# Kernel tuning notes

Measured on AMD Instinct MI355X. Metric: run time of the kernel, lower is better.

Reference implementation:

```python
import jax, jax.numpy as jnp
import numpy as np

B, L, E, H, WINDOW = 4, 1024, 1024, 16, 4
D = E // H  # head_dim = 64
SCALING = D ** -0.5


def setup_inputs() -> dict:
    key = jax.random.key(0)
    ks = jax.random.split(key, 12)
    s = E ** -0.5
    return {
        "hidden_states": jax.random.normal(ks[0], (B, L, E), dtype=jnp.float32),
        "Wq": jax.random.normal(ks[1], (E, E), dtype=jnp.float32) * s,
        "bq": jnp.zeros((E,), dtype=jnp.float32),
        "Wk": jax.random.normal(ks[2], (E, E), dtype=jnp.float32) * s,
        "bk": jnp.zeros((E,), dtype=jnp.float32),
        "Wv": jax.random.normal(ks[3], (E, E), dtype=jnp.float32) * s,
        "bv": jnp.zeros((E,), dtype=jnp.float32),
        "Wo": jax.random.normal(ks[4], (E, E), dtype=jnp.float32) * s,
        "bo": jnp.zeros((E,), dtype=jnp.float32),
        "emb_rel_k": jax.random.normal(ks[5], (1, 2 * WINDOW + 1, D), dtype=jnp.float32) * SCALING,
        "emb_rel_v": jax.random.normal(ks[6], (1, 2 * WINDOW + 1, D), dtype=jnp.float32) * SCALING,
    }


def _get_relative_embeddings(emb, length):
    # emb: (1, 2*window+1, D) -> (1, 2*length-1, D)
    pad_length = max(length - (WINDOW + 1), 0)
    if pad_length > 0:
        emb = jnp.pad(emb, ((0, 0), (pad_length, pad_length), (0, 0)))
    start = max(WINDOW + 1 - length, 0)
    return emb[:, start:start + 2 * length - 1]


def _rel_to_abs(x):
    # x: (BH, L, 2L-1) -> (BH, L, L)
    bh, length, _ = x.shape
    x = jnp.pad(x, ((0, 0), (0, 0), (0, 1)))            # (BH, L, 2L)
    xf = x.reshape(bh, length * 2 * length)
    xf = jnp.pad(xf, ((0, 0), (0, length - 1)))
    xfin = xf.reshape(bh, length + 1, 2 * length - 1)
    return xfin[:, :length, length - 1:]


def _abs_to_rel(x):
    # x: (BH, L, L) -> (BH, L, 2L-1)
    bh, length, _ = x.shape
    x = jnp.pad(x, ((0, 0), (0, 0), (0, length - 1)))    # (BH, L, 2L-1)
    xf = x.reshape(bh, length * (2 * length - 1))
    xf = jnp.pad(xf, ((0, 0), (length, 0)))
    xfin = xf.reshape(bh, length, 2 * length)
    return xfin[:, :, 1:]


def reference(hidden_states, Wq, bq, Wk, bk, Wv, bv, Wo, bo, emb_rel_k, emb_rel_v):
    bsz, tgt_len, _ = hidden_states.shape

    def shape(t):  # (B, L, E) -> (B*H, L, D)
        return t.reshape(bsz, tgt_len, H, D).transpose(0, 2, 1, 3).reshape(bsz * H, tgt_len, D)

    q = shape((hidden_states @ Wq + bq) * SCALING)
    k = shape(hidden_states @ Wk + bk)
    v = shape(hidden_states @ Wv + bv)
    src_len = k.shape[1]

    attn_weights = jnp.einsum("btd,bsd->bts", q, k)  # (BH, L, L)

    rel_k = _get_relative_embeddings(emb_rel_k, src_len)          # (1, 2L-1, D)
    rel_logits = jnp.einsum("btd,md->btm", q, rel_k[0])           # (BH, L, 2L-1)
    attn_weights = attn_weights + _rel_to_abs(rel_logits)

    attn_probs = jax.nn.softmax(attn_weights, axis=-1)

    attn_output = jnp.einsum("bts,bsd->btd", attn_probs, v)       # (BH, L, D)

    rel_v = _get_relative_embeddings(emb_rel_v, src_len)          # (1, 2L-1, D)
    rel_weights = _abs_to_rel(attn_probs)                         # (BH, L, 2L-1)
    attn_output = attn_output + jnp.einsum("btm,md->btd", rel_weights, rel_v[0])

    out = attn_output.reshape(bsz, H, tgt_len, D).transpose(0, 2, 1, 3).reshape(bsz, tgt_len, E)
    return out @ Wo + bo
```

## Files before the change

### kernel.cpp

```cpp
#include <hip/hip_runtime.h>
#include <math.h>

#define LQ 1024
#define EE 1024
#define NH 16
#define HD 64
#define SCALING 0.125f

typedef unsigned short u16;
typedef __bf16 bf16x8 __attribute__((ext_vector_type(8)));
typedef __bf16 bf16x4 __attribute__((ext_vector_type(4)));
typedef float f32x4 __attribute__((ext_vector_type(4)));

#define MFMA16(a, b, c) __builtin_amdgcn_mfma_f32_16x16x32_bf16(a, b, c, 0, 0, 0)
#define BAR() __builtin_amdgcn_s_barrier()

__device__ __forceinline__ void split_bf16(float x, __bf16& h, __bf16& l)
{
    h = (__bf16)x;
    l = (__bf16)(x - (float)h);
}

__device__ __forceinline__ u16 bf16_bits(__bf16 v)
{
    union { __bf16 b; u16 u; } cv;
    cv.b = v;
    return cv.u;
}

__global__ __launch_bounds__(256) void conv_all(
    const float* __restrict__ A,
    const float* __restrict__ Wq, const float* __restrict__ Wk,
    const float* __restrict__ Wv, const float* __restrict__ Wo,
    __bf16* __restrict__ Ah,
    __bf16* __restrict__ BTq, __bf16* __restrict__ BTk,
    __bf16* __restrict__ BTv, __bf16* __restrict__ BTo)
{
    __shared__ float tbuf[64][65];
    const int bid = blockIdx.x;
    const int tid = threadIdx.x;

    if (bid < 1024) {
        int t = bid * 256 + tid;
#pragma unroll
        for (int it = 0; it < 4; it++) {
            int f = t + it * 262144;
            int m = f >> 8, c4 = f & 255;
            float4 x = ((const float4*)A)[f];
            bf16x4 hv;
            hv[0] = (__bf16)x.x; hv[1] = (__bf16)x.y;
            hv[2] = (__bf16)x.z; hv[3] = (__bf16)x.w;
            *(bf16x4*)(Ah + (size_t)m * 1024 + c4 * 4) = hv;
        }
        return;
    }

    const int b2 = bid - 1024;
    const int z  = b2 >> 8;
    const int rem = b2 & 255;
    const int n0 = (rem & 15) * 64, k0 = (rem >> 4) * 64;
    const float* W = (z == 0) ? Wq : (z == 1) ? Wk : (z == 2) ? Wv : Wo;
    __bf16* BT     = (z == 0) ? BTq : (z == 1) ? BTk : (z == 2) ? BTv : BTo;

#pragma unroll
    for (int rr = 0; rr < 4; rr++) {
        int f = rr * 256 + tid;
        int kl = f >> 4, n4 = f & 15;
        float4 x = *(const float4*)&W[(size_t)(k0 + kl) * EE + n0 + n4 * 4];
        tbuf[kl][n4 * 4 + 0] = x.x;
        tbuf[kl][n4 * 4 + 1] = x.y;
        tbuf[kl][n4 * 4 + 2] = x.z;
        tbuf[kl][n4 * 4 + 3] = x.w;
    }
    __syncthreads();
#pragma unroll
    for (int rr = 0; rr < 2; rr++) {
        int f = rr * 256 + tid;
        int nl = f >> 3, c8 = f & 7;
        bf16x8 hv;
#pragma unroll
        for (int j = 0; j < 8; j++) hv[j] = (__bf16)tbuf[c8 * 8 + j][nl];
        *(bf16x8*)(BT + (size_t)(n0 + nl) * 1024 + k0 + c8 * 8) = hv;
    }
}

__global__ __launch_bounds__(512, 2) void qkv_mfma(
    const u16* __restrict__ Ah, const u16* __restrict__ BTall,
    const float* __restrict__ bq, const float* __restrict__ bk, const float* __restrict__ bv,
    __bf16* __restrict__ qo, __bf16* __restrict__ ko, __bf16* __restrict__ vto)
{
    const int wg   = blockIdx.x;
    const int xcd  = wg & 7, idx = wg >> 3;
    const int tile = xcd * 24 + idx;
    const int by   = tile / 12, bx = tile % 12;

    __shared__ __attribute__((aligned(16))) u16 smem[65536];
    u16 (*Ab_lds)[2][8192] = (u16(*)[2][8192])smem;
    u16 (*Bb_lds)[2][8192] = (u16(*)[2][8192])(smem + 32768);

    const int tid  = threadIdx.x;
    const int lane = tid & 63;
    const int wave = tid >> 6;
    const int wr   = wave >> 2, wc = wave & 3;
    const int rl   = lane & 15, lq = lane >> 4;

    const int m0    = by * 256;
    const int nrow0 = bx * 256;

    f32x4 acc[8][4] = {};
    bf16x8 af[2][4], bn0[2][2], bn1[2][2];

    auto stA = [&](int buf, int half, int kt) {
        int k0 = kt * 64;
#pragma unroll
        for (int it = 0; it < 2; it++) {
            int c = it * 512 + tid, k2 = c >> 7, row = c & 127;
            __builtin_amdgcn_global_load_lds(
                Ah + (size_t)(m0 + half * 128 + row) * 1024 + k0 + k2 * 8,
                &Ab_lds[buf][half][c * 8], 16, 0, 0);
        }
    };
    auto stB = [&](int buf, int half, int kt) {
        int k0 = kt * 64;
#pragma unroll
        for (int it = 0; it < 2; it++) {
            int c = it * 512 + tid, k2 = c >> 7, row = c & 127;
            __builtin_amdgcn_global_load_lds(
                BTall + (size_t)(nrow0 + half * 128 + row) * 1024 + k0 + k2 * 8,
                &Bb_lds[buf][half][c * 8], 16, 0, 0);
        }
    };
    auto rdA = [&](int buf, int mh) {
#pragma unroll
        for (int kk = 0; kk < 2; kk++)
#pragma unroll
            for (int mi = 0; mi < 4; mi++)
                af[kk][mi] = *(const bf16x8*)&Ab_lds[buf][wr]
                    [((kk * 4 + lq) * 128 + mh * 64 + mi * 16 + rl) * 8];
    };
    auto rdB = [&](int buf, int nh, bf16x8 (&bf)[2][2]) {
#pragma unroll
        for (int kk = 0; kk < 2; kk++)
#pragma unroll
            for (int ni = 0; ni < 2; ni++)
                bf[kk][ni] = *(const bf16x8*)&Bb_lds[buf][wc >> 1]
                    [((kk * 4 + lq) * 128 + (wc & 1) * 64 + nh * 32 + ni * 16 + rl) * 8];
    };
    auto mfma_q = [&](int mh, int nh, bf16x8 (&bf)[2][2]) {
        __builtin_amdgcn_s_setprio(1);
#pragma unroll
        for (int kk = 0; kk < 2; kk++)
#pragma unroll
            for (int mi = 0; mi < 4; mi++)
#pragma unroll
                for (int ni = 0; ni < 2; ni++)
                    acc[mh * 4 + mi][nh * 2 + ni] =
                        MFMA16(af[kk][mi], bf[kk][ni], acc[mh * 4 + mi][nh * 2 + ni]);
        __builtin_amdgcn_s_setprio(0);
    };

    auto body = [&](int t, bool last) {
        rdA(0, 0); rdB(0, 0, bn0);
        stA(1, 0, t + 1);
        BAR(); mfma_q(0, 0, bn0); BAR();
        rdB(0, 1, bn1);
        stA(1, 1, t + 1);
        BAR(); mfma_q(0, 1, bn1); BAR();
        rdA(0, 1);
        if (!last) stB(0, 0, t + 2);
        BAR(); mfma_q(1, 0, bn0); BAR();
        if (!last) {
            stB(0, 1, t + 2);
            asm volatile("s_waitcnt vmcnt(4)" ::: "memory");
        } else {
            asm volatile("s_waitcnt vmcnt(0)" ::: "memory");
        }
        BAR(); mfma_q(1, 1, bn1); BAR();
        rdA(1, 0); rdB(1, 0, bn0);
        if (!last) stA(0, 0, t + 2);
        BAR(); mfma_q(0, 0, bn0); BAR();
        rdB(1, 1, bn1);
        if (!last) stA(0, 1, t + 2);
        BAR(); mfma_q(0, 1, bn1); BAR();
        rdA(1, 1);
        if (!last) stB(1, 0, t + 3);
        BAR(); mfma_q(1, 0, bn0); BAR();
        if (!last) {
            stB(1, 1, t + 3);
            asm volatile("s_waitcnt vmcnt(4)" ::: "memory");
        }
        BAR(); mfma_q(1, 1, bn1); BAR();
    };

    stB(0, 0, 0); stB(0, 1, 0);
    stA(0, 0, 0); stA(0, 1, 0);
    stB(1, 0, 1); stB(1, 1, 1);
    asm volatile("s_waitcnt vmcnt(4)" ::: "memory");
    BAR();

    for (int i = 0; i < 7; i++) body(2 * i, false);
    body(14, true);

    const int z   = bx >> 2;
    const int n0l = (bx & 3) * 256;
    const float* bias = (z == 0) ? bq : (z == 1) ? bk : bv;
    const float qs    = (z == 0) ? SCALING : 1.0f;
    const int b  = m0 >> 10;
    const int t0 = m0 & 1023;

    if (z < 2) {
        __bf16* O = (z == 0) ? qo : ko;
#pragma unroll
        for (int mi = 0; mi < 8; mi++)
#pragma unroll
            for (int ni = 0; ni < 4; ni++) {
                int col = wc * 64 + ni * 16 + rl;
                float bb = bias[n0l + col];
                int c = col >> 3, j = col & 7;
#pragma unroll
                for (int r = 0; r < 4; r++) {
                    int row = wr * 128 + mi * 16 + lq * 4 + r;
                    smem[((row << 5) + (c ^ (row & 15))) * 8 + j] =
                        bf16_bits((__bf16)((acc[mi][ni][r] + bb) * qs));
                }
            }
        __syncthreads();
        const int h0 = n0l >> 6;
#pragma unroll
        for (int it = 0; it < 16; it++) {
            int id = it * 512 + tid;
            int row = id >> 5, c = id & 31;
            bf16x8 vv = *(const bf16x8*)&smem[((row << 5) + (c ^ (row & 15))) * 8];
            __bf16* dst = O + ((size_t)((b * NH + h0 + (c >> 3)) * LQ) + t0 + row) * HD
                            + (c & 7) * 8;
            *(bf16x8*)dst = vv;
        }
    } else {
#pragma unroll
        for (int mi = 0; mi < 8; mi++)
#pragma unroll
            for (int ni = 0; ni < 4; ni++) {
                int n = n0l + wc * 64 + ni * 16 + rl;
                int h = n >> 6, d = n & 63;
                float bb = bias[n];
                bf16x4 pv;
#pragma unroll
                for (int r = 0; r < 4; r++) pv[r] = (__bf16)(acc[mi][ni][r] + bb);
                int t = t0 + wr * 128 + mi * 16 + lq * 4;
                *(bf16x4*)(vto + ((size_t)(b * NH + h) * HD + d) * LQ + t) = pv;
            }
    }
}

__device__ __forceinline__ void stage_op(
    const u16* __restrict__ Ab, const u16* __restrict__ Bb,
    int m0, int nrow0, int k0, int tid, u16* As, u16* Bs)
{
#pragma unroll
    for (int it = 0; it < 2; it++) {
        int c = it * 512 + tid;
        int k2 = c >> 7, row = c & 127;
        __builtin_amdgcn_global_load_lds(Ab + (size_t)(m0 + row) * 1024 + k0 + k2 * 8,
                                         As + (size_t)c * 8, 16, 0, 0);
    }
#pragma unroll
    for (int it = 0; it < 2; it++) {
        int c = it * 512 + tid;
        int k2 = c >> 7, row = c & 127;
        __builtin_amdgcn_global_load_lds(Bb + (size_t)(nrow0 + row) * 1024 + k0 + k2 * 8,
                                         Bs + (size_t)c * 8, 16, 0, 0);
    }
}

__global__ __launch_bounds__(512) void oproj_mfma(
    const u16* __restrict__ Ao, const u16* __restrict__ BTo,
    const float* __restrict__ bo, float* __restrict__ O)
{
    const int wg  = blockIdx.x;
    const int xcd = wg & 7, idx = wg >> 3;
    const int swz = xcd * 32 + idx;
    const int by  = swz >> 3, bx = swz & 7;

    __shared__ __attribute__((aligned(16))) u16 As[2][8192], Bs[2][8192];

    const int tid  = threadIdx.x;
    const int lane = tid & 63;
    const int wave = tid >> 6;
    const int wr   = wave >> 2, wc = wave & 3;
    const int rl   = lane & 15, lq = lane >> 4;

    const int m0 = by * 128, n0 = bx * 128;

    f32x4 acc[4][2] = {};

    auto compute = [&](const u16* Ac, const u16* Bc) {
#pragma unroll
        for (int kk = 0; kk < 2; kk++) {
            bf16x8 af[4], bfr[2];
#pragma unroll
            for (int mi = 0; mi < 4; mi++)
                af[mi] = *(const bf16x8*)(Ac +
                    (size_t)((kk * 4 + lq) * 128 + wr * 64 + mi * 16 + rl) * 8);
#pragma unroll
            for (int ni = 0; ni < 2; ni++)
                bfr[ni] = *(const bf16x8*)(Bc +
                    (size_t)((kk * 4 + lq) * 128 + wc * 32 + ni * 16 + rl) * 8);
#pragma unroll
            for (int mi = 0; mi < 4; mi++)
#pragma unroll
                for (int ni = 0; ni < 2; ni++)
                    acc[mi][ni] = MFMA16(af[mi], bfr[ni], acc[mi][ni]);
        }
    };

    stage_op(Ao, BTo, m0, n0, 0,  tid, As[0], Bs[0]);
    stage_op(Ao, BTo, m0, n0, 64, tid, As[1], Bs[1]);

    int cur = 0;
    for (int i = 0; i < 15; i++) {
        asm volatile("s_waitcnt vmcnt(4)" ::: "memory");
        __builtin_amdgcn_s_barrier();
        compute(As[cur], Bs[cur]);
        asm volatile("s_waitcnt lgkmcnt(0)" ::: "memory");
        __builtin_amdgcn_s_barrier();
        if (i + 2 < 16)
            stage_op(Ao, BTo, m0, n0, (i + 2) * 64, tid, As[cur], Bs[cur]);
        cur ^= 1;
    }
    asm volatile("s_waitcnt vmcnt(0)" ::: "memory");
    __builtin_amdgcn_s_barrier();
    compute(As[cur], Bs[cur]);

#pragma unroll
    for (int mi = 0; mi < 4; mi++)
#pragma unroll
        for (int ni = 0; ni < 2; ni++) {
            int n = n0 + wc * 32 + ni * 16 + rl;
            float bb = bo[n];
#pragma unroll
            for (int r = 0; r < 4; r++) {
                int m = m0 + wr * 64 + mi * 16 + lq * 4 + r;
                O[(size_t)m * EE + n] = acc[mi][ni][r] + bb;
            }
        }
}

__device__ __forceinline__ bf16x8 ld_frag(const u16* base, int row, int col)
{
    int off = (row * 128 + col * 2) ^ ((row & 7) << 4);
    return *(const bf16x8*)((const char*)base + off);
}

__global__ __launch_bounds__(512) void attn_mfma(
    const u16* __restrict__ qb, const u16* __restrict__ kb,
    const u16* __restrict__ vtb,
    const float* __restrict__ relk, const float* __restrict__ relv,
    __bf16* __restrict__ Ao)
{
    __shared__ __attribute__((aligned(16))) u16 pool[16384];
    __shared__ __attribute__((aligned(16))) u16 k_lds[64 * 64];
    __shared__ __attribute__((aligned(16))) u16 v_lds[64 * 64];
    __shared__ float R_lds[128 * 9];
    __shared__ float rk_lds[9 * 64];
    __shared__ float rv_lds[9 * 64];

    u16* q_lds = pool;

    const int tid  = threadIdx.x;
    const int lane = tid & 63;
    const int wave = tid >> 6;
    const int rl   = lane & 15, lq = lane >> 4;
    const int bh   = blockIdx.y;
    const int q0   = blockIdx.x * 128;

#pragma unroll
    for (int rr = 0; rr < 2; rr++) {
        int f = rr * 512 + tid;
        int row = f >> 3, c8 = f & 7;
        const u16* src = qb + ((size_t)bh * LQ + q0 + row) * HD + ((c8 ^ (row & 7)) * 8);
        __builtin_amdgcn_global_load_lds(src, q_lds + (size_t)(f & ~63) * 8, 16, 0, 0);
    }
    for (int u = tid; u < 144; u += 512)
        *(float4*)&rk_lds[u * 4] = *(const float4*)&relk[u * 4];
    for (int u = tid; u < 144; u += 512)
        *(float4*)&rv_lds[u * 4] = *(const float4*)&relv[u * 4];
    __syncthreads();

    for (int j = tid; j < 1152; j += 512) {
        int tl = j / 9, i = j - tl * 9;
        float acc = 0.f;
        for (int d = 0; d < 64; d++) {
            int off = (tl * 128 + d * 2) ^ ((tl & 7) << 4);
            float qv = (float)*(const __bf16*)((const char*)q_lds + off);
            acc += qv * rk_lds[i * 64 + d];
        }
        R_lds[tl * 9 + i] = acc;
    }

    bf16x8 qa[2];
    qa[0] = ld_frag(q_lds, wave * 16 + rl, lq * 8);
    qa[1] = ld_frag(q_lds, wave * 16 + rl, 32 + lq * 8);

    __syncthreads();

    f32x4 of[4] = {};
    float l_r[4] = {0.f, 0.f, 0.f, 0.f};

    const u16* pw = pool + 8192 + wave * 1024;
    u16* pww      = pool + 8192 + wave * 1024;

    for (int s0 = 0; s0 < LQ; s0 += 64) {
        {
            int row = tid >> 3, c8 = tid & 7;
            const u16* srck = kb + ((size_t)bh * LQ + s0 + row) * HD + ((c8 ^ (row & 7)) * 8);
            __builtin_amdgcn_global_load_lds(srck, k_lds + (size_t)(tid & ~63) * 8, 16, 0, 0);
            const u16* srcv = vtb + ((size_t)bh * HD + row) * LQ + s0 + ((c8 ^ (row & 7)) * 8);
            __builtin_amdgcn_global_load_lds(srcv, v_lds + (size_t)(tid & ~63) * 8, 16, 0, 0);
        }
        __syncthreads();

        f32x4 sf[4] = {};
#pragma unroll
        for (int sub = 0; sub < 4; sub++) {
#pragma unroll
            for (int kk = 0; kk < 2; kk++) {
                bf16x8 kf = ld_frag(k_lds, sub * 16 + rl, kk * 32 + lq * 8);
                sf[sub] = MFMA16(qa[kk], kf, sf[sub]);
            }
        }

        int drel = s0 - q0;
        bool diag = (drel >= -64) && (drel <= 128);
        if (diag) {
#pragma unroll
            for (int sub = 0; sub < 4; sub++) {
#pragma unroll
                for (int r = 0; r < 4; r++) {
                    int tl = wave * 16 + lq * 4 + r;
                    int s  = s0 + sub * 16 + rl;
                    int i  = s - (q0 + tl) + 4;
                    if ((unsigned)i <= 8u) sf[sub][r] += R_lds[tl * 9 + i];
                }
            }
        }

#pragma unroll
        for (int sub = 0; sub < 4; sub++) {
#pragma unroll
            for (int r = 0; r < 4; r++) {
                float p = __expf(sf[sub][r]);
                l_r[r] += p;
                int q = lq * 4 + r;
                int off = (q * 128 + (sub * 16 + rl) * 2) ^ ((q & 7) << 4);
                *(__bf16*)((char*)pww + off) = (__bf16)p;
            }
        }

#pragma unroll
        for (int kk = 0; kk < 2; kk++) {
            bf16x8 pa = ld_frag(pw, rl, kk * 32 + lq * 8);
#pragma unroll
            for (int dsub = 0; dsub < 4; dsub++) {
                bf16x8 vf = ld_frag(v_lds, dsub * 16 + rl, kk * 32 + lq * 8);
                of[dsub] = MFMA16(pa, vf, of[dsub]);
            }
        }

        if (diag) {
#pragma unroll
            for (int r = 0; r < 4; r++) {
                int q  = lq * 4 + r;
                int tl = wave * 16 + q;
#pragma unroll
                for (int i = 0; i < 9; i++) {
                    int s  = q0 + tl + i - 4;
                    int sl = s - s0;
                    if ((unsigned)sl < 64u) {
                        int off = (q * 128 + sl * 2) ^ ((q & 7) << 4);
                        float p = (float)*(const __bf16*)((const char*)pww + off);
#pragma unroll
                        for (int dsub = 0; dsub < 4; dsub++)
                            of[dsub][r] += p * rv_lds[i * 64 + dsub * 16 + rl];
                    }
                }
            }
        }
        __syncthreads();
    }

#pragma unroll
    for (int r = 0; r < 4; r++) {
        float s = l_r[r];
#pragma unroll
        for (int msk = 8; msk >= 1; msk >>= 1) s += __shfl_xor(s, msk, 64);
        l_r[r] = 1.0f / s;
    }

#pragma unroll
    for (int dsub = 0; dsub < 4; dsub++) {
#pragma unroll
        for (int r = 0; r < 4; r++) {
            int row = wave * 16 + lq * 4 + r;
            float v = of[dsub][r] * l_r[r];
            int col = dsub * 16 + rl;
            int c = col >> 3, j = col & 7;
            pool[(row * 8 + (c ^ (row & 7))) * 8 + j] = bf16_bits((__bf16)v);
        }
    }
    __syncthreads();
    const int b = bh >> 4, h = bh & 15;
#pragma unroll
    for (int it = 0; it < 2; it++) {
        int id = it * 512 + tid;
        int row = id >> 3, c = id & 7;
        bf16x8 vv = *(const bf16x8*)&pool[(row * 8 + (c ^ (row & 7))) * 8];
        __bf16* dst = Ao + ((size_t)(b * LQ) + q0 + row) * 1024 + h * 64 + c * 8;
        *(bf16x8*)dst = vv;
    }
}

extern "C" void kernel_launch(void* const* d_in, const int* in_sizes, int n_in,
                              void* d_out, int out_size, void* d_ws, size_t ws_size,
                              hipStream_t stream)
{
    const float* hidden = (const float*)d_in[0];
    const float* Wq = (const float*)d_in[1];
    const float* bq = (const float*)d_in[2];
    const float* Wk = (const float*)d_in[3];
    const float* bk = (const float*)d_in[4];
    const float* Wv = (const float*)d_in[5];
    const float* bv = (const float*)d_in[6];
    const float* Wo = (const float*)d_in[7];
    const float* bo = (const float*)d_in[8];
    const float* relk = (const float*)d_in[9];
    const float* relv = (const float*)d_in[10];

    char* w = (char*)d_ws;
    __bf16* Ah   = (__bf16*)(w);
    __bf16* Ao   = (__bf16*)(w);
    __bf16* BTq  = (__bf16*)(w + (8u << 20));
    __bf16* BTk  = (__bf16*)(w + (10u << 20));
    __bf16* BTv  = (__bf16*)(w + (12u << 20));
    __bf16* BTo  = (__bf16*)(w + (14u << 20));
    __bf16* qbw  = (__bf16*)(w + (16u << 20));
    __bf16* kbw  = (__bf16*)(w + (24u << 20));
    __bf16* vtbw = (__bf16*)(w + (32u << 20));
    float*  out  = (float*)d_out;

    conv_all<<<2048, 256, 0, stream>>>(hidden, Wq, Wk, Wv, Wo, Ah,
                                       BTq, BTk, BTv, BTo);
    qkv_mfma<<<192, 512, 0, stream>>>((const u16*)Ah, (const u16*)BTq,
                                      bq, bk, bv, qbw, kbw, vtbw);
    attn_mfma<<<dim3(8, 64), 512, 0, stream>>>((const u16*)qbw, (const u16*)kbw,
        (const u16*)vtbw, relk, relv, Ao);
    oproj_mfma<<<256, 512, 0, stream>>>((const u16*)Ao, (const u16*)BTo, bo, out);
}
```

Measured before the change: 133.4 us.

## Stage two K/V tiles per barrier and remap attention blocks per XCD

The attention kernel now loads two 64-key K/V tiles into separate LDS buffers before one barrier, then processes both. This halves the number of barrier pairs per block and puts more loads in flight at once. The grid is also flattened to 1D and remapped so that all query blocks of the same batch-head run on the same XCD, which is meant to improve L2 reuse of K/V. In exchange, LDS use for K/V doubles and the code gets larger from the lambda-inlined loop body.

```diff
diff --git a/kernel.cpp b/kernel.cpp
--- a/kernel.cpp
+++ b/kernel.cpp
@@ -358,20 +358,30 @@
     __bf16* __restrict__ Ao)
 {
     __shared__ __attribute__((aligned(16))) u16 pool[16384];
-    __shared__ __attribute__((aligned(16))) u16 k_lds[64 * 64];
-    __shared__ __attribute__((aligned(16))) u16 v_lds[64 * 64];
+    __shared__ __attribute__((aligned(16))) u16 k_lds[2][4096];
+    __shared__ __attribute__((aligned(16))) u16 v_lds[2][4096];
     __shared__ float R_lds[128 * 9];
     __shared__ float rk_lds[9 * 64];
     __shared__ float rv_lds[9 * 64];
 
     u16* q_lds = pool;
 
-    const int tid  = threadIdx.x;
-    const int lane = tid & 63;
-    const int wave = tid >> 6;
-    const int rl   = lane & 15, lq = lane >> 4;
-    const int bh   = blockIdx.y;
-    const int q0   = blockIdx.x * 128;
+    const int tid   = threadIdx.x;
+    const int lane  = tid & 63;
+    const int wave  = tid >> 6;
+    const int rl    = lane & 15, lq = lane >> 4;
+    const int wg    = blockIdx.x;
+    const int xcd   = wg & 7, inner = wg >> 3;
+    const int bh    = xcd + 8 * (inner & 7);
+    const int q0    = (inner >> 3) * 128;
+
+    auto stage64 = [&](u16* kl, u16* vl, int s0) {
+        int row = tid >> 3, c8 = tid & 7;
+        const u16* srck = kb + ((size_t)bh * LQ + s0 + row) * HD + ((c8 ^ (row & 7)) * 8);
+        __builtin_amdgcn_global_load_lds(srck, kl + (size_t)(tid & ~63) * 8, 16, 0, 0);
+        const u16* srcv = vtb + ((size_t)bh * HD + row) * LQ + s0 + ((c8 ^ (row & 7)) * 8);
+        __builtin_amdgcn_global_load_lds(srcv, vl + (size_t)(tid & ~63) * 8, 16, 0, 0);
+    };
 
 #pragma unroll
     for (int rr = 0; rr < 2; rr++) {
@@ -409,27 +419,18 @@
     const u16* pw = pool + 8192 + wave * 1024;
     u16* pww      = pool + 8192 + wave * 1024;
 
-    for (int s0 = 0; s0 < LQ; s0 += 64) {
-        {
-            int row = tid >> 3, c8 = tid & 7;
-            const u16* srck = kb + ((size_t)bh * LQ + s0 + row) * HD + ((c8 ^ (row & 7)) * 8);
-            __builtin_amdgcn_global_load_lds(srck, k_lds + (size_t)(tid & ~63) * 8, 16, 0, 0);
-            const u16* srcv = vtb + ((size_t)bh * HD + row) * LQ + s0 + ((c8 ^ (row & 7)) * 8);
-            __builtin_amdgcn_global_load_lds(srcv, v_lds + (size_t)(tid & ~63) * 8, 16, 0, 0);
-        }
-        __syncthreads();
-
+    auto half_body = [&](const u16* kl, const u16* vl, int s0h) {
         f32x4 sf[4] = {};
 #pragma unroll
         for (int sub = 0; sub < 4; sub++) {
 #pragma unroll
             for (int kk = 0; kk < 2; kk++) {
-                bf16x8 kf = ld_frag(k_lds, sub * 16 + rl, kk * 32 + lq * 8);
+                bf16x8 kf = ld_frag(kl, sub * 16 + rl, kk * 32 + lq * 8);
                 sf[sub] = MFMA16(qa[kk], kf, sf[sub]);
             }
         }
 
-        int drel = s0 - q0;
+        int drel = s0h - q0;
         bool diag = (drel >= -64) && (drel <= 128);
         if (diag) {
 #pragma unroll
@@ -437,7 +438,7 @@
 #pragma unroll
                 for (int r = 0; r < 4; r++) {
                     int tl = wave * 16 + lq * 4 + r;
-                    int s  = s0 + sub * 16 + rl;
+                    int s  = s0h + sub * 16 + rl;
                     int i  = s - (q0 + tl) + 4;
                     if ((unsigned)i <= 8u) sf[sub][r] += R_lds[tl * 9 + i];
                 }
@@ -461,7 +462,7 @@
             bf16x8 pa = ld_frag(pw, rl, kk * 32 + lq * 8);
 #pragma unroll
             for (int dsub = 0; dsub < 4; dsub++) {
-                bf16x8 vf = ld_frag(v_lds, dsub * 16 + rl, kk * 32 + lq * 8);
+                bf16x8 vf = ld_frag(vl, dsub * 16 + rl, kk * 32 + lq * 8);
                 of[dsub] = MFMA16(pa, vf, of[dsub]);
             }
         }
@@ -474,7 +475,7 @@
 #pragma unroll
                 for (int i = 0; i < 9; i++) {
                     int s  = q0 + tl + i - 4;
-                    int sl = s - s0;
+                    int sl = s - s0h;
                     if ((unsigned)sl < 64u) {
                         int off = (q * 128 + sl * 2) ^ ((q & 7) << 4);
                         float p = (float)*(const __bf16*)((const char*)pww + off);
@@ -485,6 +486,15 @@
                 }
             }
         }
+    };
+
+    for (int c = 0; c < 8; c++) {
+        const int s0 = c * 128;
+        stage64(k_lds[0], v_lds[0], s0);
+        stage64(k_lds[1], v_lds[1], s0 + 64);
+        __syncthreads();
+        half_body(k_lds[0], v_lds[0], s0);
+        half_body(k_lds[1], v_lds[1], s0 + 64);
         __syncthreads();
     }
 
@@ -551,7 +561,7 @@
                                        BTq, BTk, BTv, BTo);
     qkv_mfma<<<192, 512, 0, stream>>>((const u16*)Ah, (const u16*)BTq,
                                       bq, bk, bv, qbw, kbw, vtbw);
-    attn_mfma<<<dim3(8, 64), 512, 0, stream>>>((const u16*)qbw, (const u16*)kbw,
+    attn_mfma<<<512, 512, 0, stream>>>((const u16*)qbw, (const u16*)kbw,
         (const u16*)vtbw, relk, relv, Ao);
     oproj_mfma<<<256, 512, 0, stream>>>((const u16*)Ao, (const u16*)BTo, bo, out);
 }
```

Result: slower. 142.7 us (+6.9%).
